# Kernel optimization log

Hardware: AMD Instinct MI355X
Metric: run time of the kernel (lower is better)

The kernel has to match this reference:

```python
import jax, jax.numpy as jnp
import numpy as np

SHAPES = ((100, 152), (50, 76), (25, 38), (13, 19))  # per-level (H, W), stride 8/16/32/64 of 800x1216
S_TOTAL = sum(h * w for h, w in SHAPES)  # 20197
D, H, LVL, P, NL, H2 = 256, 8, 4, 4, 6, 2
B, NQ_TOTAL, NPROP = 8, 350, 300
DFF = 1024


def layer_norm(x, w, b, eps=1e-5):
    m = jnp.mean(x, -1, keepdims=True)
    v = jnp.mean((x - m) ** 2, -1, keepdims=True)
    return (x - m) / jnp.sqrt(v + eps) * w + b


def pos2posemb(pos, num_pos_feats=64, temperature=10000.0):
    pos = pos * (2.0 * np.pi)
    dim_t = temperature ** (2.0 * (jnp.arange(num_pos_feats) // 2).astype(jnp.float32) / num_pos_feats)
    pe = pos[..., None] / dim_t  # [..., 4, 64]
    pe = jnp.stack((jnp.sin(pe[..., 0::2]), jnp.cos(pe[..., 1::2])), axis=-1)  # [..., 4, 32, 2]
    return pe.reshape(pe.shape[:-3] + (-1,))  # [..., 256]


def bilinear_gather(v_l, loc, hl, wl):
    # v_l [B, hl*wl, H, Dh]; loc [B, Nq, H, P, 2] in [0,1]; grid_sample align_corners=False, zero padding
    b, nq, h, p, _ = loc.shape
    dh = v_l.shape[-1]
    x = loc[..., 0] * wl - 0.5
    y = loc[..., 1] * hl - 0.5
    x0 = jnp.floor(x)
    y0 = jnp.floor(y)
    lx = x - x0
    ly = y - y0

    def g(xi, yi):
        valid = (xi >= 0) & (xi <= wl - 1) & (yi >= 0) & (yi <= hl - 1)
        xi_i = jnp.clip(xi, 0, wl - 1).astype(jnp.int32)
        yi_i = jnp.clip(yi, 0, hl - 1).astype(jnp.int32)
        idx = (yi_i * wl + xi_i).transpose(0, 1, 3, 2).reshape(b, nq * p, h)  # per-head spatial index
        out = jnp.take_along_axis(v_l, jnp.broadcast_to(idx[..., None], (b, nq * p, h, dh)), axis=1)
        out = out.reshape(b, nq, p, h, dh).transpose(0, 1, 3, 2, 4)  # [B,Nq,H,P,Dh]
        return out * valid.astype(v_l.dtype)[..., None]

    return (g(x0, y0) * ((1 - lx) * (1 - ly))[..., None]
            + g(x0 + 1, y0) * (lx * (1 - ly))[..., None]
            + g(x0, y0 + 1) * ((1 - lx) * ly)[..., None]
            + g(x0 + 1, y0 + 1) * (lx * ly)[..., None])


def ms_deform_attn(query, ref, src, Woff, boff, Wa, ba, Wv, bv, Wout, bout):
    b, nq, d = query.shape
    dh = d // H
    value = (src @ Wv + bv).reshape(b, -1, H, dh)
    off = (query @ Woff + boff).reshape(b, nq, H, LVL, P, 2)
    attn = jax.nn.softmax((query @ Wa + ba).reshape(b, nq, H, LVL * P), -1).reshape(b, nq, H, LVL, P)
    # 4-d reference points: center + offsets scaled by box size
    loc = ref[:, :, None, :, None, :2] + off / P * ref[:, :, None, :, None, 2:] * 0.5  # [b,nq,H,L,P,2]
    out = jnp.zeros((b, nq, H, dh), query.dtype)
    start = 0
    for l, (hl, wl) in enumerate(SHAPES):
        v_l = value[:, start:start + hl * wl]
        start += hl * wl
        samp = bilinear_gather(v_l, loc[:, :, :, l], hl, wl)  # [b,nq,H,P,dh]
        out = out + (samp * attn[:, :, :, l, :, None]).sum(3)
    return out.reshape(b, nq, d) @ Wout + bout


def weight_attn(q_in, k_in, Wq, bq, Wk, bk):
    b, nq, d = q_in.shape
    nk = k_in.shape[1]
    dh = d // H2
    q = (q_in @ Wq + bq).reshape(b, nq, H2, dh).transpose(0, 2, 1, 3)
    k = (k_in @ Wk + bk).reshape(b, nk, H2, dh).transpose(0, 2, 1, 3)
    mm = jax.nn.softmax(jnp.einsum('bhqd,bhkd->bhqk', q, k) * (1.0 / dh ** 0.5), -1)
    qn = q / (jnp.linalg.norm(q, axis=-1, keepdims=True) + 1e-6)
    kn = k / (jnp.linalg.norm(k, axis=-1, keepdims=True) + 1e-6)
    cos = jnp.einsum('bhqd,bhkd->bhqk', qn, kn)
    return cos, mm


def setup_inputs():
    key = jax.random.key(0)
    ks = jax.random.split(key, 32)
    f = jnp.float32
    inp = {}
    inp['tgt'] = jax.random.normal(ks[0], (B, NQ_TOTAL, D), f)
    inp['reference_points'] = jax.random.uniform(ks[1], (B, NQ_TOTAL, 4), f, 0.05, 0.95)
    inp['src'] = jax.random.normal(ks[2], (B, S_TOTAL, D), f)
    inp['src_spatial_shapes'] = jnp.array(SHAPES, jnp.int32)
    lsi = np.cumsum([0] + [h * w for h, w in SHAPES])[:-1]
    inp['src_level_start_index'] = jnp.array(lsi, jnp.int32)
    inp['src_valid_ratios'] = jnp.ones((B, LVL, 2), f)
    inp['num_proposals'] = NPROP
    names = [('Woff', (NL, D, H * LVL * P * 2)), ('boff', (NL, H * LVL * P * 2)),
             ('Wa', (NL, D, H * LVL * P)), ('ba', (NL, H * LVL * P)),
             ('Wv', (NL, D, D)), ('bv', (NL, D)), ('Wout', (NL, D, D)), ('bout', (NL, D)),
             ('Wl1', (NL, D, DFF)), ('bl1', (NL, DFF)), ('Wl2', (NL, DFF, D)), ('bl2', (NL, D)),
             ('Wq', (NL, D, D)), ('bq', (NL, D)), ('Wk', (NL, D, D)), ('bk', (NL, D))]
    for i, (n, s) in enumerate(names):
        inp[n] = jax.random.normal(ks[3 + i], s, f) * 0.02
    inp['n1w'] = jnp.ones((NL, D), f)
    inp['n1b'] = jnp.zeros((NL, D), f)
    inp['n3w'] = jnp.ones((NL, D), f)
    inp['n3b'] = jnp.zeros((NL, D), f)
    return inp


def reference(tgt, reference_points, src, src_spatial_shapes, src_level_start_index,
              src_valid_ratios, num_proposals, Woff, boff, Wa, ba, Wv, bv, Wout, bout,
              Wl1, bl1, Wl2, bl2, Wq, bq, Wk, bk, n1w, n1b, n3w, n3b):
    proposals = tgt[:, :num_proposals]
    track_queries = tgt[:, num_proposals:]
    p_ref = reference_points[:, :num_proposals]
    t_ref = reference_points[:, num_proposals:]
    vr = jnp.concatenate([src_valid_ratios, src_valid_ratios], -1)  # [B,L,4]
    ref_input = p_ref[:, :, None] * vr[:, None]  # [B,Np,L,4]
    p_pos = pos2posemb(p_ref)
    t_pos = pos2posemb(t_ref)  # computed per torch code; WeightAttention ignores pos
    for l in range(NL):
        q = proposals + p_pos
        ca = ms_deform_attn(q, ref_input, src, Woff[l], boff[l], Wa[l], ba[l], Wv[l], bv[l], Wout[l], bout[l])
        proposals = layer_norm(proposals + ca, n1w[l], n1b[l])  # dropout = identity (eval)
        ffn = jax.nn.relu(proposals @ Wl1[l] + bl1[l]) @ Wl2[l] + bl2[l]
        proposals = layer_norm(proposals + ffn, n3w[l], n3b[l])
        pt_cos, pt_mm = weight_attn(proposals, track_queries, Wq[l], bq[l], Wk[l], bk[l])
        pp_cos, pp_mm = weight_attn(proposals, proposals, Wq[l], bq[l], Wk[l], bk[l])
    return proposals, p_ref, pt_cos, pp_cos, pt_mm, pp_mm
```

## Files before the change

kernel.cpp:

```cpp
#include <hip/hip_runtime.h>

#define BB 8
#define NQ 300
#define NTQ 50
#define NLAY 6
#define S_TOTAL 20197
#define ROWS (BB*NQ)
#define MVAL (BB*S_TOTAL)

typedef unsigned short u16;
typedef unsigned int u32;
typedef __bf16 v8bf __attribute__((ext_vector_type(8)));
typedef float f32x4 __attribute__((ext_vector_type(4)));

__device__ __forceinline__ u16 f2b(float f) {
    u32 u = __float_as_uint(f);
    u32 r = (u + 0x7fffu + ((u >> 16) & 1u)) >> 16;
    return (u16)r;
}
__device__ __forceinline__ u32 pk2(float lo, float hi) {
    return (u32)f2b(lo) | ((u32)f2b(hi) << 16);
}

#define ASYNC_CP16(dst_lds, src_g) \
    __builtin_amdgcn_global_load_lds((const __attribute__((address_space(1))) u32*)(src_g), \
                                     (__attribute__((address_space(3))) u32*)(dst_lds), 16, 0, 0)

__global__ void transpose_pack(
    const float* Woff, const float* Wa, const float* Wv, const float* Wout,
    const float* Wl1, const float* Wl2, const float* Wq, const float* Wk,
    const float* boff, const float* ba, const float* bvp, const float* bout,
    const float* bl1, const float* bl2, const float* bq, const float* bk,
    u16* wt, float* bias)
{
    int idx = blockIdx.x * 256 + threadIdx.x;
    if (idx < 5308416) {
        int l = idx / 884736;
        int o = idx % 884736;
        float v;
        if (o < 98304) { int n = o >> 8, k = o & 255;
            v = (n < 256) ? Woff[l*65536 + k*256 + n] : Wa[l*32768 + k*128 + (n-256)];
        } else if (o < 163840) { int o2 = o - 98304; int n = o2 >> 8, k = o2 & 255;
            v = Wv[l*65536 + k*256 + n];
        } else if (o < 229376) { int o2 = o - 163840; int n = o2 >> 8, k = o2 & 255;
            v = Wout[l*65536 + k*256 + n];
        } else if (o < 491520) { int o2 = o - 229376; int n = o2 >> 8, k = o2 & 255;
            v = Wl1[l*262144 + k*1024 + n];
        } else if (o < 753664) { int o2 = o - 491520; int n = o2 >> 10, k = o2 & 1023;
            v = Wl2[l*262144 + k*256 + n];
        } else { int o2 = o - 753664; int n = o2 >> 8, k = o2 & 255;
            v = (n < 256) ? Wq[l*65536 + k*256 + n] : Wk[l*65536 + k*256 + (n-256)];
        }
        wt[idx] = f2b(v);
    } else {
        int i2 = idx - 5308416;
        if (i2 < 16128) {
            int l = i2 / 2688, o = i2 % 2688;
            float v;
            if (o < 256)       v = boff[l*256 + o];
            else if (o < 384)  v = ba  [l*128 + (o-256)];
            else if (o < 640)  v = bvp [l*256 + (o-384)];
            else if (o < 896)  v = bout[l*256 + (o-640)];
            else if (o < 1920) v = bl1 [l*1024 + (o-896)];
            else if (o < 2176) v = bl2 [l*256 + (o-1920)];
            else if (o < 2432) v = bq  [l*256 + (o-2176)];
            else               v = bk  [l*256 + (o-2432)];
            bias[i2] = v;
        }
    }
}

__global__ void src_convert(const float* __restrict__ src, u16* __restrict__ dst)
{
    long i = ((long)blockIdx.x*256 + threadIdx.x)*8;
    float4 a = *(const float4*)(src+i), b4 = *(const float4*)(src+i+4);
    uint4 o = make_uint4(pk2(a.x,a.y), pk2(a.z,a.w), pk2(b4.x,b4.y), pk2(b4.z,b4.w));
    *(uint4*)&dst[i] = o;
}

__global__ void setup_kernel(const float* tgt, const float* refp, float* prop,
                             u16* q_b, float* ppos, u16* tq, float* out_pref)
{
    int row = blockIdx.x, t = threadIdx.x;
    if (row < ROWS) {
        int b = row / NQ, q = row % NQ;
        int k = t >> 6, rem = t & 63, j = rem >> 1;
        float pr = refp[(b*350 + q)*4 + k];
        float dimt = powf(10000.0f, (float)j * (1.0f/32.0f));
        float arg = pr * 6.283185307179586f / dimt;
        float pe = (rem & 1) ? cosf(arg) : sinf(arg);
        ppos[row*256 + t] = pe;
        float pv = tgt[(b*350 + q)*256 + t];
        prop[row*256 + t] = pv;
        q_b[row*256 + t] = f2b(pv + pe);
        if (t < 4) out_pref[row*4 + t] = refp[(b*350 + q)*4 + t];
    } else {
        int r2 = row - ROWS;
        int b = r2 / NTQ, qq = r2 % NTQ;
        tq[r2*256 + t] = f2b(tgt[(b*350 + NQ + qq)*256 + t]);
    }
}

__global__ __launch_bounds__(256) void gemm_bt(
    const u16* __restrict__ A, const u16* __restrict__ Bt,
    const float* __restrict__ bias, void* __restrict__ Cout,
    int M, int N, int K, int flags)
{
    __shared__ __align__(16) u16 As[2][128*32];
    __shared__ __align__(16) u16 Bs[2][128*32];
    int tid = threadIdx.x;
    int lane = tid & 63, wave = tid >> 6;
    int bm = blockIdx.y * 128, bn = blockIdx.x * 128;
    int wm = (wave >> 1) * 64, wn = (wave & 1) * 64;
    f32x4 acc[4][4] = {};
    int r = tid >> 2, c = (tid & 3) * 8;
    const u16* Ap0 = A  + (long)min(bm + r,      M-1) * K + c;
    const u16* Ap1 = A  + (long)min(bm + r + 64, M-1) * K + c;
    const u16* Bp0 = Bt + (long)min(bn + r,      N-1) * K + c;
    const u16* Bp1 = Bt + (long)min(bn + r + 64, N-1) * K + c;
    int fr = lane & 15, fk = (lane >> 4) * 8;

    auto STG = [&](int bi, int k0) {
        ASYNC_CP16(&As[bi][tid*8],         Ap0 + k0);
        ASYNC_CP16(&As[bi][64*32 + tid*8], Ap1 + k0);
        ASYNC_CP16(&Bs[bi][tid*8],         Bp0 + k0);
        ASYNC_CP16(&Bs[bi][64*32 + tid*8], Bp1 + k0);
    };
    STG(0, 0);
    asm volatile("s_waitcnt vmcnt(0)" ::: "memory");
    __syncthreads();
    int cur = 0;
    for (int k0 = 0; k0 < K; k0 += 32) {
        if (k0 + 32 < K) STG(cur ^ 1, k0 + 32);
        v8bf af[4], bf[4];
        #pragma unroll
        for (int i = 0; i < 4; ++i) af[i] = *(const v8bf*)&As[cur][(wm + i*16 + fr)*32 + fk];
        #pragma unroll
        for (int j = 0; j < 4; ++j) bf[j] = *(const v8bf*)&Bs[cur][(wn + j*16 + fr)*32 + fk];
        #pragma unroll
        for (int i = 0; i < 4; ++i)
            #pragma unroll
            for (int j = 0; j < 4; ++j)
                acc[i][j] = __builtin_amdgcn_mfma_f32_16x16x32_bf16(af[i], bf[j], acc[i][j], 0, 0, 0);
        asm volatile("s_waitcnt vmcnt(0)" ::: "memory");
        __syncthreads();
        cur ^= 1;
    }
    int cq = lane >> 4, cn = lane & 15;
    #pragma unroll
    for (int i = 0; i < 4; ++i) {
        #pragma unroll
        for (int j = 0; j < 4; ++j) {
            int col = bn + wn + j*16 + cn;
            float bv_ = bias ? bias[col] : 0.0f;
            #pragma unroll
            for (int rr = 0; rr < 4; ++rr) {
                int m = bm + wm + i*16 + cq*4 + rr;
                if (m < M) {
                    float v = acc[i][j][rr] + bv_;
                    if (flags & 1) v = fmaxf(v, 0.0f);
                    if (flags & 2) ((u16*)Cout)[(long)m*N + col] = f2b(v);
                    else           ((float*)Cout)[(long)m*N + col] = v;
                }
            }
        }
    }
}

__global__ __launch_bounds__(256) void gemm_bt64(
    const u16* __restrict__ A, const u16* __restrict__ Bt,
    const float* __restrict__ bias, void* __restrict__ Cout,
    int M, int N, int K, int flags)
{
    __shared__ __align__(16) u16 As[2][64*32];
    __shared__ __align__(16) u16 Bs[2][128*32];
    int tid = threadIdx.x;
    int lane = tid & 63, wave = tid >> 6;
    int bm = blockIdx.y * 64, bn = blockIdx.x * 128;
    int wm = (wave >> 1) * 32, wn = (wave & 1) * 64;
    f32x4 acc[2][4] = {};
    int r = tid >> 2, c = (tid & 3) * 8;
    const u16* Ap0 = A  + (long)min(bm + r,      M-1) * K + c;
    const u16* Bp0 = Bt + (long)min(bn + r,      N-1) * K + c;
    const u16* Bp1 = Bt + (long)min(bn + r + 64, N-1) * K + c;
    int fr = lane & 15, fk = (lane >> 4) * 8;

    auto STG = [&](int bi, int k0) {
        ASYNC_CP16(&As[bi][tid*8],         Ap0 + k0);
        ASYNC_CP16(&Bs[bi][tid*8],         Bp0 + k0);
        ASYNC_CP16(&Bs[bi][64*32 + tid*8], Bp1 + k0);
    };
    STG(0, 0);
    asm volatile("s_waitcnt vmcnt(0)" ::: "memory");
    __syncthreads();
    int cur = 0;
    for (int k0 = 0; k0 < K; k0 += 32) {
        if (k0 + 32 < K) STG(cur ^ 1, k0 + 32);
        v8bf af[2], bf[4];
        #pragma unroll
        for (int i = 0; i < 2; ++i) af[i] = *(const v8bf*)&As[cur][(wm + i*16 + fr)*32 + fk];
        #pragma unroll
        for (int j = 0; j < 4; ++j) bf[j] = *(const v8bf*)&Bs[cur][(wn + j*16 + fr)*32 + fk];
        #pragma unroll
        for (int i = 0; i < 2; ++i)
            #pragma unroll
            for (int j = 0; j < 4; ++j)
                acc[i][j] = __builtin_amdgcn_mfma_f32_16x16x32_bf16(af[i], bf[j], acc[i][j], 0, 0, 0);
        asm volatile("s_waitcnt vmcnt(0)" ::: "memory");
        __syncthreads();
        cur ^= 1;
    }
    int cq = lane >> 4, cn = lane & 15;
    #pragma unroll
    for (int i = 0; i < 2; ++i) {
        #pragma unroll
        for (int j = 0; j < 4; ++j) {
            int col = bn + wn + j*16 + cn;
            float bv_ = bias ? bias[col] : 0.0f;
            #pragma unroll
            for (int rr = 0; rr < 4; ++rr) {
                int m = bm + wm + i*16 + cq*4 + rr;
                if (m < M) {
                    float v = acc[i][j][rr] + bv_;
                    if (flags & 1) v = fmaxf(v, 0.0f);
                    if (flags & 2) ((u16*)Cout)[(long)m*N + col] = f2b(v);
                    else           ((float*)Cout)[(long)m*N + col] = v;
                }
            }
        }
    }
}

__global__ __launch_bounds__(256) void gemm_value6(
    const u16* __restrict__ A, const u16* __restrict__ wtall,
    const float* __restrict__ biasall, u16* __restrict__ Cout)
{
    __shared__ __align__(16) u16 As[2][128*32];
    __shared__ __align__(16) u16 Bs[2][128*32];
    const int nwg = 12*1263;
    int bid = blockIdx.x;
    int q_ = nwg >> 3, r_ = nwg & 7;
    int xcd = bid & 7, sl = bid >> 3;
    int wgid = (xcd < r_ ? xcd*(q_+1) : r_*(q_+1) + (xcd - r_)*q_) + sl;
    int y = wgid / 12, zx = wgid - y*12;
    int z = zx >> 1;
    int bm = y*128, bn = (zx & 1)*128;
    const u16* Bt = wtall + (size_t)z*884736 + 98304;
    const float* bs = biasall + z*2688 + 384;
    u16* Cz = Cout + (size_t)z*((size_t)MVAL*256);

    int tid = threadIdx.x;
    int lane = tid & 63, wave = tid >> 6;
    int wm = (wave >> 1) * 64, wn = (wave & 1) * 64;
    f32x4 acc[4][4] = {};
    int r = tid >> 2, c = (tid & 3) * 8;
    const u16* Ap0 = A  + (long)min(bm + r,      MVAL-1) * 256 + c;
    const u16* Ap1 = A  + (long)min(bm + r + 64, MVAL-1) * 256 + c;
    const u16* Bp0 = Bt + (long)(bn + r)      * 256 + c;
    const u16* Bp1 = Bt + (long)(bn + r + 64) * 256 + c;
    int fr = lane & 15, fk = (lane >> 4) * 8;

    auto STG = [&](int bi, int k0) {
        ASYNC_CP16(&As[bi][tid*8],         Ap0 + k0);
        ASYNC_CP16(&As[bi][64*32 + tid*8], Ap1 + k0);
        ASYNC_CP16(&Bs[bi][tid*8],         Bp0 + k0);
        ASYNC_CP16(&Bs[bi][64*32 + tid*8], Bp1 + k0);
    };
    STG(0, 0);
    asm volatile("s_waitcnt vmcnt(0)" ::: "memory");
    __syncthreads();
    int cur = 0;
    for (int k0 = 0; k0 < 256; k0 += 32) {
        if (k0 + 32 < 256) STG(cur ^ 1, k0 + 32);
        v8bf af[4], bf[4];
        #pragma unroll
        for (int i = 0; i < 4; ++i) af[i] = *(const v8bf*)&As[cur][(wm + i*16 + fr)*32 + fk];
        #pragma unroll
        for (int j = 0; j < 4; ++j) bf[j] = *(const v8bf*)&Bs[cur][(wn + j*16 + fr)*32 + fk];
        #pragma unroll
        for (int i = 0; i < 4; ++i)
            #pragma unroll
            for (int j = 0; j < 4; ++j)
                acc[i][j] = __builtin_amdgcn_mfma_f32_16x16x32_bf16(af[i], bf[j], acc[i][j], 0, 0, 0);
        asm volatile("s_waitcnt vmcnt(0)" ::: "memory");
        __syncthreads();
        cur ^= 1;
    }
    int cq = lane >> 4, cn = lane & 15;
    #pragma unroll
    for (int i = 0; i < 4; ++i) {
        #pragma unroll
        for (int j = 0; j < 4; ++j) {
            int col = bn + wn + j*16 + cn;
            float bv_ = bs[col];
            #pragma unroll
            for (int rr = 0; rr < 4; ++rr) {
                int m = bm + wm + i*16 + cq*4 + rr;
                if (m < MVAL)
                    Cz[(long)m*256 + col] = f2b(acc[i][j][rr] + bv_);
            }
        }
    }
}

__global__ __launch_bounds__(256) void sample_fused(
    const u16* __restrict__ value, const float* __restrict__ offatt,
    const float* __restrict__ refp, const float* __restrict__ svr,
    u16* __restrict__ sampout)
{
    int row = blockIdx.x, t = threadIdx.x;
    int b = row / NQ, q = row % NQ;
    __shared__ float lg[128], awl[128], sxl[128], syl[128];
    const int WL[4] = {152,76,38,19}, HL[4] = {100,50,25,13}, LS[4] = {0,15200,19000,19950};

    if (t < 128) lg[t] = offatt[row*384 + 256 + t];
    __syncthreads();
    if (t < 128) {
        int h = t >> 4, s = t & 15, lvl = s >> 2, pp = s & 3;
        int gb = h << 4;
        float mx = -1e30f;
        for (int i = 0; i < 16; ++i) mx = fmaxf(mx, lg[gb + i]);
        float sm = 0.f;
        for (int i = 0; i < 16; ++i) sm += expf(lg[gb + i] - mx);
        awl[t] = expf(lg[t] - mx) / sm;
        float rx = refp[(b*350+q)*4 + 0] * svr[(b*4+lvl)*2 + 0];
        float ry = refp[(b*350+q)*4 + 1] * svr[(b*4+lvl)*2 + 1];
        float rw = refp[(b*350+q)*4 + 2] * svr[(b*4+lvl)*2 + 0];
        float rh = refp[(b*350+q)*4 + 3] * svr[(b*4+lvl)*2 + 1];
        float ox = offatt[row*384 + h*32 + lvl*8 + pp*2 + 0];
        float oy = offatt[row*384 + h*32 + lvl*8 + pp*2 + 1];
        sxl[t] = (rx + ox * 0.25f * rw * 0.5f) * (float)WL[lvl] - 0.5f;
        syl[t] = (ry + oy * 0.25f * rh * 0.5f) * (float)HL[lvl] - 0.5f;
    }
    __syncthreads();

    int lane = t & 63, wv = t >> 6;
    int g = lane >> 3, e = lane & 7;
    for (int hh = 0; hh < 2; ++hh) {
        int h = wv*2 + hh;
        float a0 = 0.f, a1 = 0.f, a2 = 0.f, a3 = 0.f;
        #pragma unroll
        for (int it = 0; it < 8; ++it) {
            int task = it*8 + g;
            int s = task >> 2, cc = task & 3;
            int cx = cc & 1, cy = cc >> 1;
            int lvl = s >> 2;
            float x = sxl[h*16 + s], y2 = syl[h*16 + s], aw = awl[h*16 + s];
            float x0 = floorf(x), y0 = floorf(y2);
            float xc = x0 + (float)cx, yc = y0 + (float)cy;
            int wl = WL[lvl], hl = HL[lvl];
            if (xc >= 0.f && xc <= (float)(wl-1) && yc >= 0.f && yc <= (float)(hl-1)) {
                float lx = x - x0, ly = y2 - y0;
                float wgt = aw * (cx ? lx : 1.f - lx) * (cy ? ly : 1.f - ly);
                long off = ((long)b*S_TOTAL + LS[lvl] + (int)yc*wl + (int)xc)*256 + h*32 + e*4;
                uint2 v = *(const uint2*)(value + off);
                a0 += wgt * __uint_as_float((v.x & 0xffffu) << 16);
                a1 += wgt * __uint_as_float(v.x & 0xffff0000u);
                a2 += wgt * __uint_as_float((v.y & 0xffffu) << 16);
                a3 += wgt * __uint_as_float(v.y & 0xffff0000u);
            }
        }
        #pragma unroll
        for (int o = 8; o < 64; o <<= 1) {
            a0 += __shfl_xor(a0, o); a1 += __shfl_xor(a1, o);
            a2 += __shfl_xor(a2, o); a3 += __shfl_xor(a3, o);
        }
        if (g == 0)
            *(uint2*)&sampout[row*256 + h*32 + e*4] = make_uint2(pk2(a0, a1), pk2(a2, a3));
    }
}

__global__ void ln_kernel(float* __restrict__ prop, const float* __restrict__ delta,
                          const float* __restrict__ w, const float* __restrict__ bsh,
                          u16* __restrict__ pb_out, u16* __restrict__ q_out,
                          const float* __restrict__ ppos)
{
    int row = blockIdx.x, t = threadIdx.x;
    int lane = t & 63, wv = t >> 6;
    float v = prop[row*256 + t] + delta[row*256 + t];
    float s = v;
    for (int o = 32; o; o >>= 1) s += __shfl_xor(s, o);
    __shared__ float red[4], red2[4];
    if (lane == 0) red[wv] = s;
    __syncthreads();
    float mean = (red[0]+red[1]+red[2]+red[3]) * (1.0f/256.0f);
    float dd = v - mean;
    float s2 = dd * dd;
    for (int o = 32; o; o >>= 1) s2 += __shfl_xor(s2, o);
    if (lane == 0) red2[wv] = s2;
    __syncthreads();
    float var = (red2[0]+red2[1]+red2[2]+red2[3]) * (1.0f/256.0f);
    float nv = dd * rsqrtf(var + 1e-5f) * w[t] + bsh[t];
    prop[row*256 + t] = nv;
    pb_out[row*256 + t] = f2b(nv);
    if (q_out) q_out[row*256 + t] = f2b(nv + ppos[row*256 + t]);
}

__global__ __launch_bounds__(128) void qk_convert(
    const float* __restrict__ qkp, const float* __restrict__ kt,
    u16* __restrict__ qk_b, u16* __restrict__ kt_b,
    float* __restrict__ qn_g, float* __restrict__ knp_g, float* __restrict__ knt_g)
{
    int row = blockIdx.x, t = threadIdx.x;
    __shared__ float part[128];
    if (row < ROWS) {
        const float* sp = qkp + (long)row*512 + t*4;
        float4 v = *(const float4*)sp;
        *(uint2*)&qk_b[(long)row*512 + t*4] = make_uint2(pk2(v.x,v.y), pk2(v.z,v.w));
        part[t] = v.x*v.x + v.y*v.y + v.z*v.z + v.w*v.w;
        __syncthreads();
        if (t < 4) {
            float s = 0.f;
            for (int i = 0; i < 32; ++i) s += part[t*32 + i];
            int b = row / NQ, q = row % NQ;
            float nv = sqrtf(s) + 1e-6f;
            if      (t == 0) qn_g [(b*2+0)*NQ + q] = nv;
            else if (t == 1) qn_g [(b*2+1)*NQ + q] = nv;
            else if (t == 2) knp_g[(b*2+0)*NQ + q] = nv;
            else             knp_g[(b*2+1)*NQ + q] = nv;
        }
    } else {
        int r2 = row - ROWS;
        float ss = 0.f;
        if (t < 64) {
            const float* sp = kt + (long)r2*256 + t*4;
            float4 v = *(const float4*)sp;
            *(uint2*)&kt_b[(long)r2*256 + t*4] = make_uint2(pk2(v.x,v.y), pk2(v.z,v.w));
            ss = v.x*v.x + v.y*v.y + v.z*v.z + v.w*v.w;
        }
        part[t] = ss;
        __syncthreads();
        if (t < 2) {
            float s = 0.f;
            for (int i = 0; i < 32; ++i) s += part[t*32 + i];
            int b = r2 / NTQ, qq = r2 % NTQ;
            knt_g[(b*2+t)*NTQ + qq] = sqrtf(s) + 1e-6f;
        }
    }
}

__global__ __launch_bounds__(256) void wattn_mfma(
    const u16* __restrict__ Qb, const u16* __restrict__ Kb,
    int qstride, int kstride, int koff, int nk,
    const float* __restrict__ qn_g, const float* __restrict__ kn_g,
    float* __restrict__ out_cos, float* __restrict__ out_logit)
{
    __shared__ __align__(16) u16 As[2][128*32];
    __shared__ __align__(16) u16 Bs[2][128*32];
    int bh = blockIdx.z, b = bh >> 1, h = bh & 1;
    int tid = threadIdx.x;
    int lane = tid & 63, wave = tid >> 6;
    int bm = blockIdx.y * 128, bn = blockIdx.x * 128;
    int wm = (wave >> 1) * 64, wn = (wave & 1) * 64;
    f32x4 acc[4][4] = {};
    int r = tid >> 2, c = (tid & 3) * 8;
    const u16* Ap0 = Qb + (long)(b*NQ + min(bm + r,      NQ-1))*qstride + h*128 + c;
    const u16* Ap1 = Qb + (long)(b*NQ + min(bm + r + 64, NQ-1))*qstride + h*128 + c;
    const u16* Bp0 = Kb + (long)(b*nk + min(bn + r,      nk-1))*kstride + koff + h*128 + c;
    const u16* Bp1 = Kb + (long)(b*nk + min(bn + r + 64, nk-1))*kstride + koff + h*128 + c;
    int fr = lane & 15, fk = (lane >> 4) * 8;

    auto STG = [&](int bi, int k0) {
        ASYNC_CP16(&As[bi][tid*8],         Ap0 + k0);
        ASYNC_CP16(&As[bi][64*32 + tid*8], Ap1 + k0);
        ASYNC_CP16(&Bs[bi][tid*8],         Bp0 + k0);
        ASYNC_CP16(&Bs[bi][64*32 + tid*8], Bp1 + k0);
    };
    STG(0, 0);
    asm volatile("s_waitcnt vmcnt(0)" ::: "memory");
    __syncthreads();
    int cur = 0;
    for (int k0 = 0; k0 < 128; k0 += 32) {
        if (k0 + 32 < 128) STG(cur ^ 1, k0 + 32);
        v8bf af[4], bf[4];
        #pragma unroll
        for (int i = 0; i < 4; ++i) af[i] = *(const v8bf*)&As[cur][(wm + i*16 + fr)*32 + fk];
        #pragma unroll
        for (int j = 0; j < 4; ++j) bf[j] = *(const v8bf*)&Bs[cur][(wn + j*16 + fr)*32 + fk];
        #pragma unroll
        for (int i = 0; i < 4; ++i)
            #pragma unroll
            for (int j = 0; j < 4; ++j)
                acc[i][j] = __builtin_amdgcn_mfma_f32_16x16x32_bf16(af[i], bf[j], acc[i][j], 0, 0, 0);
        asm volatile("s_waitcnt vmcnt(0)" ::: "memory");
        __syncthreads();
        cur ^= 1;
    }
    const float SC = 0.08838834764831845f;
    int cq = lane >> 4, cn = lane & 15;
    #pragma unroll
    for (int i = 0; i < 4; ++i) {
        #pragma unroll
        for (int j = 0; j < 4; ++j) {
            int col = bn + wn + j*16 + cn;
            #pragma unroll
            for (int rr = 0; rr < 4; ++rr) {
                int m = bm + wm + i*16 + cq*4 + rr;
                if (m < NQ && col < nk) {
                    float d = acc[i][j][rr];
                    long o = ((long)(bh*NQ + m))*nk + col;
                    out_cos[o]   = d / (qn_g[bh*NQ + m] * kn_g[bh*nk + col]);
                    out_logit[o] = d * SC;
                }
            }
        }
    }
}

__global__ __launch_bounds__(64) void row_softmax(float* __restrict__ buf, int nk)
{
    long row = blockIdx.x;
    float* p = buf + row*nk;
    int lane = threadIdx.x;
    float mx = -1e30f;
    for (int k = lane; k < nk; k += 64) mx = fmaxf(mx, p[k]);
    for (int o = 32; o; o >>= 1) mx = fmaxf(mx, __shfl_xor(mx, o));
    float s = 0.f;
    for (int k = lane; k < nk; k += 64) s += expf(p[k] - mx);
    for (int o = 32; o; o >>= 1) s += __shfl_xor(s, o);
    float inv = 1.0f / s;
    for (int k = lane; k < nk; k += 64) p[k] = expf(p[k] - mx) * inv;
}

__global__ void writeout_kernel(const float* __restrict__ prop, float* __restrict__ out)
{
    int row = blockIdx.x, t = threadIdx.x;
    out[row*256 + t] = prop[row*256 + t];
}

extern "C" void kernel_launch(void* const* d_in, const int* in_sizes, int n_in,
                              void* d_out, int out_size, void* d_ws, size_t ws_size,
                              hipStream_t stream)
{
    (void)in_sizes; (void)n_in; (void)out_size; (void)ws_size;
    const float* tgt  = (const float*)d_in[0];
    const float* refp = (const float*)d_in[1];
    const float* src  = (const float*)d_in[2];
    const float* svr  = (const float*)d_in[5];
    const float* Woff = (const float*)d_in[7];
    const float* boff = (const float*)d_in[8];
    const float* Wa   = (const float*)d_in[9];
    const float* ba   = (const float*)d_in[10];
    const float* Wv   = (const float*)d_in[11];
    const float* bv   = (const float*)d_in[12];
    const float* Wout = (const float*)d_in[13];
    const float* bout = (const float*)d_in[14];
    const float* Wl1  = (const float*)d_in[15];
    const float* bl1  = (const float*)d_in[16];
    const float* Wl2  = (const float*)d_in[17];
    const float* bl2  = (const float*)d_in[18];
    const float* Wq   = (const float*)d_in[19];
    const float* bq   = (const float*)d_in[20];
    const float* Wk   = (const float*)d_in[21];
    const float* bk   = (const float*)d_in[22];
    const float* n1w  = (const float*)d_in[23];
    const float* n1b  = (const float*)d_in[24];
    const float* n3w  = (const float*)d_in[25];
    const float* n3b  = (const float*)d_in[26];
    float* out = (float*)d_out;

    char* p = (char*)d_ws;
    auto alloc = [&](size_t bytes) { void* r = (void*)p; p += (bytes + 255) & ~(size_t)255; return r; };
    u16*   wt      = (u16*)  alloc(6ull*884736*2);
    float* bias    = (float*)alloc(6ull*2688*4);
    u16*   value   = (u16*)  alloc(6ull*MVAL*256*2);
    u16*   src_b   = (u16*)  alloc((size_t)MVAL*256*2);
    float* prop    = (float*)alloc((size_t)ROWS*256*4);
    u16*   prop_b  = (u16*)  alloc((size_t)ROWS*256*2);
    u16*   q_b     = (u16*)  alloc((size_t)ROWS*256*2);
    float* ppos    = (float*)alloc((size_t)ROWS*256*4);
    float* offatt  = (float*)alloc((size_t)ROWS*384*4);
    u16*   sampout = (u16*)  alloc((size_t)ROWS*256*2);
    float* ca      = (float*)alloc((size_t)ROWS*256*4);
    u16*   ff1     = (u16*)  alloc((size_t)ROWS*1024*2);
    float* ff2     = (float*)alloc((size_t)ROWS*256*4);
    u16*   tq      = (u16*)  alloc(400ull*256*2);
    float* qkp     = (float*)alloc((size_t)ROWS*512*4);
    float* kt      = (float*)alloc(400ull*256*4);
    u16*   qk_b    = (u16*)  alloc((size_t)ROWS*512*2);
    u16*   kt_b    = (u16*)  alloc(400ull*256*2);
    float* qn_g    = (float*)alloc(16ull*NQ*4);
    float* knp_g   = (float*)alloc(16ull*NQ*4);
    float* knt_g   = (float*)alloc(16ull*NTQ*4);

    transpose_pack<<<20799, 256, 0, stream>>>(Woff, Wa, Wv, Wout, Wl1, Wl2, Wq, Wk,
                                              boff, ba, bv, bout, bl1, bl2, bq, bk, wt, bias);
    src_convert<<<20197, 256, 0, stream>>>(src, src_b);
    setup_kernel<<<ROWS + 400, 256, 0, stream>>>(tgt, refp, prop, q_b, ppos, tq, out + 614400);
    gemm_value6<<<12*1263, 256, 0, stream>>>(src_b, wt, bias, value);

    for (int l = 0; l < NLAY; ++l) {
        const u16* wl_ = wt + (size_t)l*884736;
        const float* bl_ = bias + l*2688;
        gemm_bt64<<<dim3(3, 38), 256, 0, stream>>>(q_b,    wl_,          bl_,        offatt, ROWS, 384, 256, 0);
        sample_fused<<<ROWS, 256, 0, stream>>>(value + (size_t)l*MVAL*256, offatt, refp, svr, sampout);
        gemm_bt64<<<dim3(2, 38), 256, 0, stream>>>(sampout, wl_ + 163840, bl_ + 640,  ca,    ROWS, 256, 256, 0);
        ln_kernel<<<ROWS, 256, 0, stream>>>(prop, ca, n1w + l*256, n1b + l*256, prop_b, (u16*)nullptr, ppos);
        gemm_bt64<<<dim3(8, 38), 256, 0, stream>>>(prop_b, wl_ + 229376, bl_ + 896,  ff1,   ROWS, 1024, 256, 3);
        gemm_bt64<<<dim3(2, 38), 256, 0, stream>>>(ff1,    wl_ + 491520, bl_ + 1920, ff2,   ROWS, 256, 1024, 0);
        ln_kernel<<<ROWS, 256, 0, stream>>>(prop, ff2, n3w + l*256, n3b + l*256, prop_b, q_b, ppos);
    }

    const u16* w5 = wt + 5ull*884736;
    const float* b5 = bias + 5*2688;
    gemm_bt64<<<dim3(4, 38), 256, 0, stream>>>(prop_b, w5 + 753664,         b5 + 2176,       qkp, ROWS, 512, 256, 0);
    gemm_bt64<<<dim3(2, 7),  256, 0, stream>>>(tq,     w5 + 753664 + 65536, b5 + 2176 + 256, kt,  400,  256, 256, 0);
    qk_convert<<<2800, 128, 0, stream>>>(qkp, kt, qk_b, kt_b, qn_g, knp_g, knt_g);
    wattn_mfma<<<dim3(1, 3, 16), 256, 0, stream>>>(qk_b, kt_b, 512, 256, 0,   NTQ, qn_g, knt_g,
                                                   out + 624000, out + 2304000);
    wattn_mfma<<<dim3(3, 3, 16), 256, 0, stream>>>(qk_b, qk_b, 512, 512, 256, NQ,  qn_g, knp_g,
                                                   out + 864000, out + 2544000);
    row_softmax<<<4800, 64, 0, stream>>>(out + 2304000, NTQ);
    row_softmax<<<4800, 64, 0, stream>>>(out + 2544000, NQ);
    writeout_kernel<<<ROWS, 256, 0, stream>>>(prop, out);
}
```

Measured before the change: 1.300 ms.

## Restructure value-projection GEMM to keep full weight slice in LDS and stream A from global

Result: slower. 1.586 ms (+22.0%).

```diff
diff --git a/kernel.cpp b/kernel.cpp
--- a/kernel.cpp
+++ b/kernel.cpp
@@ -231,73 +231,72 @@
     }
 }
 
-__global__ __launch_bounds__(256) void gemm_value6(
+__global__ __launch_bounds__(256, 2) void gemm_value6_v2(
     const u16* __restrict__ A, const u16* __restrict__ wtall,
     const float* __restrict__ biasall, u16* __restrict__ Cout)
 {
-    __shared__ __align__(16) u16 As[2][128*32];
-    __shared__ __align__(16) u16 Bs[2][128*32];
-    const int nwg = 12*1263;
+    __shared__ __align__(16) u16 Bsw[8*4*128*8];
     int bid = blockIdx.x;
-    int q_ = nwg >> 3, r_ = nwg & 7;
     int xcd = bid & 7, sl = bid >> 3;
-    int wgid = (xcd < r_ ? xcd*(q_+1) : r_*(q_+1) + (xcd - r_)*q_) + sl;
-    int y = wgid / 12, zx = wgid - y*12;
-    int z = zx >> 1;
-    int bm = y*128, bn = (zx & 1)*128;
+    int wgid = xcd*474 + sl;
+    int rg = wgid / 12, zx = wgid % 12;
+    int z = zx >> 1, half = zx & 1;
+    int bn = half*128;
+    long rowbase0 = (long)rg * 512;
     const u16* Bt = wtall + (size_t)z*884736 + 98304;
     const float* bs = biasall + z*2688 + 384;
     u16* Cz = Cout + (size_t)z*((size_t)MVAL*256);
 
     int tid = threadIdx.x;
-    int lane = tid & 63, wave = tid >> 6;
-    int wm = (wave >> 1) * 64, wn = (wave & 1) * 64;
-    f32x4 acc[4][4] = {};
-    int r = tid >> 2, c = (tid & 3) * 8;
-    const u16* Ap0 = A  + (long)min(bm + r,      MVAL-1) * 256 + c;
-    const u16* Ap1 = A  + (long)min(bm + r + 64, MVAL-1) * 256 + c;
-    const u16* Bp0 = Bt + (long)(bn + r)      * 256 + c;
-    const u16* Bp1 = Bt + (long)(bn + r + 64) * 256 + c;
-    int fr = lane & 15, fk = (lane >> 4) * 8;
-
-    auto STG = [&](int bi, int k0) {
-        ASYNC_CP16(&As[bi][tid*8],         Ap0 + k0);
-        ASYNC_CP16(&As[bi][64*32 + tid*8], Ap1 + k0);
-        ASYNC_CP16(&Bs[bi][tid*8],         Bp0 + k0);
-        ASYNC_CP16(&Bs[bi][64*32 + tid*8], Bp1 + k0);
-    };
-    STG(0, 0);
+    int lane = tid & 63;
+    int wave = tid >> 6;
+    int fr = lane & 15, q = lane >> 4;
+
+    #pragma unroll
+    for (int it = 0; it < 16; ++it) {
+        int c_id = it*256 + tid;
+        int col   = c_id & 127;
+        int chunk = (c_id >> 7) & 3;
+        int ks    = c_id >> 9;
+        const u16* srcp = Bt + (size_t)(bn + col)*256 + ks*32 + chunk*8;
+        ASYNC_CP16(&Bsw[(size_t)c_id*8], srcp);
+    }
     asm volatile("s_waitcnt vmcnt(0)" ::: "memory");
     __syncthreads();
-    int cur = 0;
-    for (int k0 = 0; k0 < 256; k0 += 32) {
-        if (k0 + 32 < 256) STG(cur ^ 1, k0 + 32);
-        v8bf af[4], bf[4];
-        #pragma unroll
-        for (int i = 0; i < 4; ++i) af[i] = *(const v8bf*)&As[cur][(wm + i*16 + fr)*32 + fk];
-        #pragma unroll
-        for (int j = 0; j < 4; ++j) bf[j] = *(const v8bf*)&Bs[cur][(wn + j*16 + fr)*32 + fk];
-        #pragma unroll
-        for (int i = 0; i < 4; ++i)
-            #pragma unroll
-            for (int j = 0; j < 4; ++j)
-                acc[i][j] = __builtin_amdgcn_mfma_f32_16x16x32_bf16(af[i], bf[j], acc[i][j], 0, 0, 0);
-        asm volatile("s_waitcnt vmcnt(0)" ::: "memory");
-        __syncthreads();
-        cur ^= 1;
-    }
-    int cq = lane >> 4, cn = lane & 15;
+
+    float bcache[8];
     #pragma unroll
-    for (int i = 0; i < 4; ++i) {
-        #pragma unroll
-        for (int j = 0; j < 4; ++j) {
-            int col = bn + wn + j*16 + cn;
-            float bv_ = bs[col];
+    for (int j = 0; j < 8; ++j) bcache[j] = bs[bn + j*16 + fr];
+
+    for (int rt = 0; rt < 4; ++rt) {
+        long rowb = rowbase0 + rt*128 + wave*32;
+        const u16* Arow0 = A + (long)min(rowb + fr,      (long)(MVAL-1))*256 + q*8;
+        const u16* Arow1 = A + (long)min(rowb + 16 + fr, (long)(MVAL-1))*256 + q*8;
+        f32x4 acc[2][8] = {};
+        #pragma unroll
+        for (int ks = 0; ks < 8; ++ks) {
+            v8bf a0 = *(const v8bf*)(Arow0 + ks*32);
+            v8bf a1 = *(const v8bf*)(Arow1 + ks*32);
+            v8bf bf[8];
+            #pragma unroll
+            for (int j = 0; j < 8; ++j)
+                bf[j] = *(const v8bf*)&Bsw[ks*4096 + q*1024 + (j*16 + fr)*8];
+            #pragma unroll
+            for (int j = 0; j < 8; ++j) {
+                acc[0][j] = __builtin_amdgcn_mfma_f32_16x16x32_bf16(a0, bf[j], acc[0][j], 0, 0, 0);
+                acc[1][j] = __builtin_amdgcn_mfma_f32_16x16x32_bf16(a1, bf[j], acc[1][j], 0, 0, 0);
+            }
+        }
+        #pragma unroll
+        for (int j = 0; j < 8; ++j) {
+            int col = bn + j*16 + fr;
+            float bv_ = bcache[j];
             #pragma unroll
             for (int rr = 0; rr < 4; ++rr) {
-                int m = bm + wm + i*16 + cq*4 + rr;
-                if (m < MVAL)
-                    Cz[(long)m*256 + col] = f2b(acc[i][j][rr] + bv_);
+                long m0 = rowb + q*4 + rr;
+                long m1 = rowb + 16 + q*4 + rr;
+                if (m0 < MVAL) Cz[m0*256 + col] = f2b(acc[0][j][rr] + bv_);
+                if (m1 < MVAL) Cz[m1*256 + col] = f2b(acc[1][j][rr] + bv_);
             }
         }
     }
@@ -587,7 +586,7 @@
                                               boff, ba, bv, bout, bl1, bl2, bq, bk, wt, bias);
     src_convert<<<20197, 256, 0, stream>>>(src, src_b);
     setup_kernel<<<ROWS + 400, 256, 0, stream>>>(tgt, refp, prop, q_b, ppos, tq, out + 614400);
-    gemm_value6<<<12*1263, 256, 0, stream>>>(src_b, wt, bias, value);
+    gemm_value6_v2<<<3792, 256, 0, stream>>>(src_b, wt, bias, value);
 
     for (int l = 0; l < NLAY; ++l) {
         const u16* wl_ = wt + (size_t)l*884736;
```
